# Performance work log

Measured on AMD Instinct MI355X. Metric: run time of the kernel, lower is better.

## Reference

```python
import jax, jax.numpy as jnp
import numpy as np

NEG_SLOPE = 0.2  # PyG GATConv default leaky_relu slope

N_NODES = 50000
N_EDGES = 800000
IN_DIM = 128
HID = 32
HEADS = 4


def setup_inputs() -> dict:
    key = jax.random.key(0)
    ks = jax.random.split(key, 12)
    x = jax.random.normal(ks[0], (N_NODES, IN_DIM), dtype=jnp.float32)
    edge_index = jax.random.randint(ks[1], (2, N_EDGES), 0, N_NODES, dtype=jnp.int64)
    s1 = 1.0 / np.sqrt(IN_DIM)
    s2 = 1.0 / np.sqrt(HID * HEADS)
    return {
        "x": x,
        "edge_index": edge_index,
        # layer 1: GATConv(IN_DIM -> HID, heads=HEADS, concat=True)
        "W1": jax.random.normal(ks[2], (IN_DIM, HEADS * HID), dtype=jnp.float32) * s1,
        "a_src1": jax.random.normal(ks[3], (HEADS, HID), dtype=jnp.float32) * s1,
        "a_dst1": jax.random.normal(ks[4], (HEADS, HID), dtype=jnp.float32) * s1,
        "b1": jnp.zeros((HEADS * HID,), dtype=jnp.float32),
        # head: GATConv(HEADS*HID -> 1, heads=1, concat=False)
        "W2": jax.random.normal(ks[5], (HEADS * HID, 1), dtype=jnp.float32) * s2,
        "a_src2": jax.random.normal(ks[6], (1, 1), dtype=jnp.float32) * s2,
        "a_dst2": jax.random.normal(ks[7], (1, 1), dtype=jnp.float32) * s2,
        "b2": jnp.zeros((1,), dtype=jnp.float32),
    }


def gat_conv(x, src, dst, W, a_src, a_dst, b, heads, out_ch, concat, n_nodes):
    # linear transform -> [N, H, C]
    h = (x @ W).reshape(n_nodes, heads, out_ch)
    # per-node attention halves -> [N, H]
    alpha_s = jnp.einsum('nhc,hc->nh', h, a_src)
    alpha_d = jnp.einsum('nhc,hc->nh', h, a_dst)
    # per-edge logits (gather), leaky relu -> [E, H]
    e = jax.nn.leaky_relu(alpha_s[src] + alpha_d[dst], NEG_SLOPE)
    # segment softmax over destination neighborhoods
    m = jax.ops.segment_max(e, dst, num_segments=n_nodes)  # [N, H]
    m = jnp.where(jnp.isfinite(m), m, 0.0)
    ex = jnp.exp(e - m[dst])
    denom = jax.ops.segment_sum(ex, dst, num_segments=n_nodes)  # [N, H]
    alpha = ex / (denom[dst] + 1e-16)  # [E, H]
    # weighted scatter-aggregate of source messages
    msg = h[src] * alpha[:, :, None]  # [E, H, C]
    out = jax.ops.segment_sum(msg, dst, num_segments=n_nodes)  # [N, H, C]
    out = out.reshape(n_nodes, heads * out_ch) if concat else out.mean(axis=1)
    return out + b


def reference(x, edge_index, W1, a_src1, a_dst1, b1, W2, a_src2, a_dst2, b2):
    n = x.shape[0]
    # PyG GATConv adds self-loops by default
    loops = jnp.arange(n, dtype=edge_index.dtype)
    src = jnp.concatenate([edge_index[0], loops])
    dst = jnp.concatenate([edge_index[1], loops])
    h = gat_conv(x, src, dst, W1, a_src1, a_dst1, b1, HEADS, HID, True, n)
    h = jax.nn.elu(h)  # dropout inactive in eval mode
    out = gat_conv(h, src, dst, W2, a_src2, a_dst2, b2, 1, 1, False, n)
    return out.squeeze(-1)  # [N]
```

## Files before the change

kernel.cpp:

```cpp
#include <hip/hip_runtime.h>
#include <hip/hip_bf16.h>
#include <hip/hip_fp16.h>

#define N_NODES 50000
#define N_EDGES 800000
#define E_TOT   850000
#define GBLK 64
#define GEMM_BLOCKS 782
#define NR 196
#define EPB 4096
#define BIN_BLOCKS 208
#define SEGCAP 8192

__global__ __launch_bounds__(512) void bin_kernel(const int* __restrict__ ei,
                                                  int* __restrict__ rangeCursor,
                                                  unsigned* __restrict__ gseg) {
    __shared__ int cnt[NR];
    __shared__ int gbase[NR];
    const int tid = threadIdx.x;

    for (int i = tid; i < NR; i += 512) cnt[i] = 0;
    __syncthreads();

    int e0 = blockIdx.x * EPB + tid * 8;
    bool valid = (e0 < E_TOT);
    int src[8], dst[8], rg[8], rk[8];
    if (valid) {
        if (e0 < N_EDGES) {
            int4 a = *(const int4*)(ei + e0);
            int4 b = *(const int4*)(ei + e0 + 4);
            int4 c = *(const int4*)(ei + N_EDGES + e0);
            int4 d = *(const int4*)(ei + N_EDGES + e0 + 4);
            src[0]=a.x; src[1]=a.y; src[2]=a.z; src[3]=a.w;
            src[4]=b.x; src[5]=b.y; src[6]=b.z; src[7]=b.w;
            dst[0]=c.x; dst[1]=c.y; dst[2]=c.z; dst[3]=c.w;
            dst[4]=d.x; dst[5]=d.y; dst[6]=d.z; dst[7]=d.w;
        } else {
#pragma unroll
            for (int k = 0; k < 8; k++) { src[k] = dst[k] = e0 + k - N_EDGES; }
        }
#pragma unroll
        for (int k = 0; k < 8; k++) {
            rg[k] = dst[k] >> 8;
            rk[k] = atomicAdd(&cnt[rg[k]], 1);
        }
    }
    __syncthreads();
    for (int i = tid; i < NR; i += 512) {
        int c = cnt[i];
        gbase[i] = c ? atomicAdd(&rangeCursor[i], c) : 0;
    }
    __syncthreads();
    if (valid) {
#pragma unroll
        for (int k = 0; k < 8; k++) {
            int pos = gbase[rg[k]] + rk[k];
            if (pos < SEGCAP)
                gseg[(size_t)rg[k] * SEGCAP + pos] =
                    ((unsigned)(dst[k] & 255) << 17) | (unsigned)src[k];
        }
    }
}

__global__ __launch_bounds__(512) void fatgf_kernel(const int* __restrict__ rangeCursor,
                                                    const unsigned* __restrict__ gseg,
                                                    int* __restrict__ offs,
                                                    int* __restrict__ bucket,
                                                    const float* __restrict__ x,
                                                    const float* __restrict__ W1,
                                                    const float* __restrict__ asrc1,
                                                    const float* __restrict__ adst1,
                                                    __half* __restrict__ h1,
                                                    float* __restrict__ as1,
                                                    float* __restrict__ ad1) {
    __shared__ __align__(16) char smem[(1024 + SEGCAP) * 4];
    const int tid = threadIdx.x;

    if (blockIdx.x < NR) {
        int* rsc  = (int*)smem;
        int* cnt  = rsc + 256;
        int* csc  = cnt + 256;
        int* cur  = csc + 256;
        int* lbuf = cur + 256;
        const int r = blockIdx.x;

        if (tid < 256) rsc[tid] = (tid < NR) ? min(rangeCursor[tid], SEGCAP) : 0;
        __syncthreads();
        for (int d = 1; d < 256; d <<= 1) {
            int u = (tid < 256 && tid >= d) ? rsc[tid - d] : 0;
            __syncthreads();
            if (tid < 256) rsc[tid] += u;
            __syncthreads();
        }
        const int n = min(rangeCursor[r], SEGCAP);
        const int rbase = rsc[r] - n;
        const unsigned* __restrict__ seg = gseg + (size_t)r * SEGCAP;

        if (tid < 256) cnt[tid] = 0;
        __syncthreads();
        for (int i = tid; i < n; i += 512)
            atomicAdd(&cnt[seg[i] >> 17], 1);
        __syncthreads();
        if (tid < 256) csc[tid] = cnt[tid];
        __syncthreads();
        for (int d = 1; d < 256; d <<= 1) {
            int u = (tid < 256 && tid >= d) ? csc[tid - d] : 0;
            __syncthreads();
            if (tid < 256) csc[tid] += u;
            __syncthreads();
        }
        if (tid < 256) {
            int lofs = csc[tid] - cnt[tid];
            cur[tid] = lofs;
            int node = r * 256 + tid;
            if (node < N_NODES) offs[node] = rbase + lofs;
        }
        if (r == NR - 1 && tid == 0) offs[N_NODES] = rbase + n;
        __syncthreads();
        for (int i = tid; i < n; i += 512) {
            unsigned en = seg[i];
            int p = atomicAdd(&cur[en >> 17], 1);
            lbuf[p] = (int)(en & 0x1FFFFu);
        }
        __syncthreads();
        for (int i = tid; i < n; i += 512)
            bucket[rbase + i] = lbuf[i];
        return;
    }

    float* xs    = (float*)smem;
    float* sredA = xs + 32 * 65;
    float* sredB = sredA + 8 * 64;

    const int lane = tid & 63;
    const int w    = tid >> 6;
    const int head = __builtin_amdgcn_readfirstlane(w >> 1);
    const int ch   = __builtin_amdgcn_readfirstlane(w & 1);
    const int base = (blockIdx.x - NR) * GBLK;
    const int node = base + lane;

    const float* __restrict__ wh = W1 + head * 32 + ch * 16;

    float acc[16];
#pragma unroll
    for (int j = 0; j < 16; j++) acc[j] = 0.f;

    for (int kt = 0; kt < 4; kt++) {
        __syncthreads();
        {
            int row = tid >> 3, c4 = tid & 7;
            int n2 = base + row;
            float4 v = make_float4(0.f, 0.f, 0.f, 0.f);
            if (n2 < N_NODES)
                v = *(const float4*)(x + (size_t)n2 * 128 + kt * 32 + c4 * 4);
            xs[(c4 * 4 + 0) * 65 + row] = v.x;
            xs[(c4 * 4 + 1) * 65 + row] = v.y;
            xs[(c4 * 4 + 2) * 65 + row] = v.z;
            xs[(c4 * 4 + 3) * 65 + row] = v.w;
        }
        __syncthreads();

#pragma unroll 4
        for (int kk = 0; kk < 32; kk++) {
            float xv = xs[kk * 65 + lane];
            const float* __restrict__ wr = wh + (size_t)(kt * 32 + kk) * 128;
#pragma unroll
            for (int j = 0; j < 16; j++)
                acc[j] += xv * wr[j];
        }
    }

    if (node < N_NODES) {
        __half2 hp[8];
#pragma unroll
        for (int j = 0; j < 8; j++)
            hp[j] = __floats2half2_rn(acc[2 * j], acc[2 * j + 1]);
        float4* dst = (float4*)(h1 + (size_t)node * 128 + head * 32 + ch * 16);
        dst[0] = ((float4*)hp)[0];
        dst[1] = ((float4*)hp)[1];
    }

    float sa = 0.f, da = 0.f;
#pragma unroll
    for (int j = 0; j < 16; j++) {
        float v = acc[j];
        sa += v * asrc1[head * 32 + ch * 16 + j];
        da += v * adst1[head * 32 + ch * 16 + j];
    }
    sredA[w * 64 + lane] = sa;
    sredB[w * 64 + lane] = da;
    __syncthreads();
    if (tid < 256) {
        int hh = tid >> 6;
        int nd = base + lane;
        if (nd < N_NODES) {
            as1[nd * 4 + hh] = sredA[(hh * 2) * 64 + lane] + sredA[(hh * 2 + 1) * 64 + lane];
            ad1[nd * 4 + hh] = sredB[(hh * 2) * 64 + lane] + sredB[(hh * 2 + 1) * 64 + lane];
        }
    }
}

__global__ __launch_bounds__(256) void agg1_kernel(const __half* __restrict__ h1,
                                                   const float* __restrict__ as1,
                                                   const float* __restrict__ ad1,
                                                   const int* __restrict__ offs,
                                                   const int* __restrict__ bucket,
                                                   const float* __restrict__ b1,
                                                   const float* __restrict__ W2,
                                                   float* __restrict__ h2s) {
    __shared__ int   sbuf[4][64];
    __shared__ float exbuf[4][64][4];

    int w = threadIdx.x >> 6, l = threadIdx.x & 63;
    int node = blockIdx.x * 4 + w;
    if (node >= N_NODES) return;
    int sub = l & 15;
    int ep  = l >> 4;
    int head = sub >> 2;
    int a = offs[node];
    int deg = offs[node + 1] - a;
    float4 adv = *(const float4*)(ad1 + (size_t)node * 4);

    float c[8];
#pragma unroll
    for (int k = 0; k < 8; k++) c[k] = 0.f;
    float sx = 0.f;

    for (int base = 0; base < deg; base += 64) {
        int cd = min(deg - base, 64);
        {
            bool v = l < cd;
            int s = bucket[a + base + (v ? l : 0)];
            sbuf[w][l] = s;
            float4 asv = *(const float4*)(as1 + (size_t)s * 4);
            float e0 = asv.x + adv.x, e1 = asv.y + adv.y;
            float e2 = asv.z + adv.z, e3 = asv.w + adv.w;
            e0 = fmaxf(e0, 0.2f * e0);
            e1 = fmaxf(e1, 0.2f * e1);
            e2 = fmaxf(e2, 0.2f * e2);
            e3 = fmaxf(e3, 0.2f * e3);
            float4 exv;
            exv.x = v ? __expf(e0) : 0.f;
            exv.y = v ? __expf(e1) : 0.f;
            exv.z = v ? __expf(e2) : 0.f;
            exv.w = v ? __expf(e3) : 0.f;
            *(float4*)&exbuf[w][l][0] = exv;
        }
        __builtin_amdgcn_wave_barrier();
        for (int g = 0; g < cd; g += 4) {
            int j = g + ep;
            bool v2 = j < cd;
            int jj = v2 ? j : 0;
            int s = sbuf[w][jj];
            float ex = exbuf[w][jj][head];
            if (!v2) ex = 0.f;
            float4 hv = *(const float4*)(h1 + (size_t)s * 128 + sub * 8);
            const __half2* hh = (const __half2*)&hv;
            float2 f0 = __half22float2(hh[0]);
            float2 f1 = __half22float2(hh[1]);
            float2 f2 = __half22float2(hh[2]);
            float2 f3 = __half22float2(hh[3]);
            sx += ex;
            c[0] += ex * f0.x; c[1] += ex * f0.y;
            c[2] += ex * f1.x; c[3] += ex * f1.y;
            c[4] += ex * f2.x; c[5] += ex * f2.y;
            c[6] += ex * f3.x; c[7] += ex * f3.y;
        }
        __builtin_amdgcn_wave_barrier();
    }

#pragma unroll
    for (int k = 0; k < 8; k++) {
        c[k] += __shfl_xor(c[k], 16, 64);
        c[k] += __shfl_xor(c[k], 32, 64);
    }
    sx += __shfl_xor(sx, 16, 64);
    sx += __shfl_xor(sx, 32, 64);

    float r = 1.f / (sx + 1e-16f);
    float4 blo = ((const float4*)b1)[sub * 2];
    float4 bhi = ((const float4*)b1)[sub * 2 + 1];
    float4 wlo = ((const float4*)W2)[sub * 2];
    float4 whi = ((const float4*)W2)[sub * 2 + 1];
    float ob[8] = {blo.x, blo.y, blo.z, blo.w, bhi.x, bhi.y, bhi.z, bhi.w};
    float ow[8] = {wlo.x, wlo.y, wlo.z, wlo.w, whi.x, whi.y, whi.z, whi.w};
    float p = 0.f;
#pragma unroll
    for (int k = 0; k < 8; k++) {
        float o = c[k] * r + ob[k];
        float el = (o > 0.f) ? o : (__expf(o) - 1.f);
        p += el * ow[k];
    }
    p += __shfl_xor(p, 1, 64);
    p += __shfl_xor(p, 2, 64);
    p += __shfl_xor(p, 4, 64);
    p += __shfl_xor(p, 8, 64);
    if (l == 0) h2s[node] = p;
}

__global__ __launch_bounds__(256) void agg2_kernel(const float* __restrict__ h2s,
                                                   const int* __restrict__ offs,
                                                   const int* __restrict__ bucket,
                                                   const float* __restrict__ asrc2,
                                                   const float* __restrict__ adst2,
                                                   const float* __restrict__ b2,
                                                   float* __restrict__ out) {
    int w = threadIdx.x >> 6, l = threadIdx.x & 63;
    int node = blockIdx.x * 4 + w;
    if (node >= N_NODES) return;
    float asc = asrc2[0], adc = adst2[0], bias = b2[0];
    float adn = h2s[node] * adc;
    int a = offs[node], b = offs[node + 1];
    float sx = 0.f, sw = 0.f;
    for (int i = a + l; i < b; i += 64) {
        float hs = h2s[bucket[i]];
        float e = hs * asc + adn;
        e = fmaxf(e, 0.2f * e);
        float ex = __expf(e);
        sx += ex;
        sw += ex * hs;
    }
#pragma unroll
    for (int o = 32; o > 0; o >>= 1) {
        sx += __shfl_xor(sx, o, 64);
        sw += __shfl_xor(sw, o, 64);
    }
    if (l == 0) out[node] = sw / (sx + 1e-16f) + bias;
}


extern "C" void kernel_launch(void* const* d_in, const int* in_sizes, int n_in,
                              void* d_out, int out_size, void* d_ws, size_t ws_size,
                              hipStream_t stream) {
    const float* x     = (const float*)d_in[0];
    const int*   ei    = (const int*)d_in[1];
    const float* W1    = (const float*)d_in[2];
    const float* asrc1 = (const float*)d_in[3];
    const float* adst1 = (const float*)d_in[4];
    const float* b1    = (const float*)d_in[5];
    const float* W2    = (const float*)d_in[6];
    const float* asrc2 = (const float*)d_in[7];
    const float* adst2 = (const float*)d_in[8];
    const float* b2    = (const float*)d_in[9];
    float* out = (float*)d_out;

    char* ws = (char*)d_ws;
    size_t o = 0;
    auto alloc = [&](size_t bytes) -> void* {
        void* p = ws + o;
        o += (bytes + 255) & ~(size_t)255;
        return p;
    };
    int* offs    = (int*)alloc((size_t)(N_NODES + 1) * 4);
    int* bucket  = (int*)alloc((size_t)E_TOT * 4);
    __half* h1   = (__half*)alloc((size_t)N_NODES * 128 * 2);
    float* as1   = (float*)alloc((size_t)N_NODES * 4 * 4);
    float* ad1   = (float*)alloc((size_t)N_NODES * 4 * 4);
    float* h2s   = (float*)alloc((size_t)N_NODES * 4);
    int* rangeCursor = (int*)alloc((size_t)NR * 4);
    unsigned* gseg   = (unsigned*)alloc((size_t)NR * SEGCAP * 4);

    hipMemsetAsync(rangeCursor, 0, (size_t)NR * 4, stream);

    bin_kernel<<<BIN_BLOCKS, 512, 0, stream>>>(ei, rangeCursor, gseg);

    fatgf_kernel<<<NR + GEMM_BLOCKS, 512, 0, stream>>>(
        rangeCursor, gseg, offs, bucket,
        x, W1, asrc1, adst1, h1, as1, ad1);

    agg1_kernel<<<(N_NODES + 3) / 4, 256, 0, stream>>>(
        h1, as1, ad1, offs, bucket, b1, W2, h2s);

    agg2_kernel<<<(N_NODES + 3) / 4, 256, 0, stream>>>(
        h2s, offs, bucket, asrc2, adst2, b2, out);
}
```

Baseline: 99.04 us.

## Compute layer-1 projection with fp16 MFMA using a transposed fp16 weight copy

Replaces the scalar FP32 GEMM (x @ W1) in the fused kernel with __builtin_amdgcn_mfma_f32_32x32x16_f16 on 32-node tiles, converting x to fp16 on the fly. A transposed fp16 copy of W1 is built by extra blocks appended to the bin kernel, and results are staged in shared memory to write h1 and compute the per-head attention dots. Aims to cut ALU time of the dense projection, but rounds x and W1 to fp16 before accumulation and leaves half of each 512-thread GEMM block idle.

```diff
diff --git a/kernel.cpp b/kernel.cpp
--- a/kernel.cpp
+++ b/kernel.cpp
@@ -5,19 +5,32 @@
 #define N_NODES 50000
 #define N_EDGES 800000
 #define E_TOT   850000
-#define GBLK 64
-#define GEMM_BLOCKS 782
+#define GBLK 32
+#define GEMM_BLOCKS 1563
 #define NR 196
 #define EPB 4096
 #define BIN_BLOCKS 208
+#define WT_BLOCKS 32
 #define SEGCAP 8192
+
+typedef _Float16 half8 __attribute__((ext_vector_type(8)));
+typedef float f32x16 __attribute__((ext_vector_type(16)));
 
 __global__ __launch_bounds__(512) void bin_kernel(const int* __restrict__ ei,
                                                   int* __restrict__ rangeCursor,
-                                                  unsigned* __restrict__ gseg) {
+                                                  unsigned* __restrict__ gseg,
+                                                  const float* __restrict__ W1,
+                                                  _Float16* __restrict__ Wt) {
     __shared__ int cnt[NR];
     __shared__ int gbase[NR];
     const int tid = threadIdx.x;
+
+    if (blockIdx.x >= BIN_BLOCKS) {
+        int k = (blockIdx.x - BIN_BLOCKS) * 4 + (tid >> 7);
+        int c = tid & 127;
+        Wt[c * 128 + k] = (_Float16)W1[k * 128 + c];
+        return;
+    }
 
     for (int i = tid; i < NR; i += 512) cnt[i] = 0;
     __syncthreads();
@@ -67,7 +80,7 @@
                                                     int* __restrict__ offs,
                                                     int* __restrict__ bucket,
                                                     const float* __restrict__ x,
-                                                    const float* __restrict__ W1,
+                                                    const _Float16* __restrict__ Wt,
                                                     const float* __restrict__ asrc1,
                                                     const float* __restrict__ adst1,
                                                     __half* __restrict__ h1,
@@ -128,74 +141,70 @@
         return;
     }
 
-    float* xs    = (float*)smem;
-    float* sredA = xs + 32 * 65;
-    float* sredB = sredA + 8 * 64;
-
-    const int lane = tid & 63;
+    if (tid >= 256) return;
+
+    _Float16* hl = (_Float16*)smem;
+    const int l    = tid & 63;
     const int w    = tid >> 6;
-    const int head = __builtin_amdgcn_readfirstlane(w >> 1);
-    const int ch   = __builtin_amdgcn_readfirstlane(w & 1);
+    const int g    = l >> 5;
+    const int cl   = l & 31;
+    const int col  = 32 * w + cl;
     const int base = (blockIdx.x - NR) * GBLK;
-    const int node = base + lane;
-
-    const float* __restrict__ wh = W1 + head * 32 + ch * 16;
-
-    float acc[16];
-#pragma unroll
-    for (int j = 0; j < 16; j++) acc[j] = 0.f;
-
-    for (int kt = 0; kt < 4; kt++) {
-        __syncthreads();
-        {
-            int row = tid >> 3, c4 = tid & 7;
-            int n2 = base + row;
-            float4 v = make_float4(0.f, 0.f, 0.f, 0.f);
-            if (n2 < N_NODES)
-                v = *(const float4*)(x + (size_t)n2 * 128 + kt * 32 + c4 * 4);
-            xs[(c4 * 4 + 0) * 65 + row] = v.x;
-            xs[(c4 * 4 + 1) * 65 + row] = v.y;
-            xs[(c4 * 4 + 2) * 65 + row] = v.z;
-            xs[(c4 * 4 + 3) * 65 + row] = v.w;
-        }
-        __syncthreads();
-
-#pragma unroll 4
-        for (int kk = 0; kk < 32; kk++) {
-            float xv = xs[kk * 65 + lane];
-            const float* __restrict__ wr = wh + (size_t)(kt * 32 + kk) * 128;
-#pragma unroll
-            for (int j = 0; j < 16; j++)
-                acc[j] += xv * wr[j];
-        }
-    }
-
-    if (node < N_NODES) {
-        __half2 hp[8];
-#pragma unroll
-        for (int j = 0; j < 8; j++)
-            hp[j] = __floats2half2_rn(acc[2 * j], acc[2 * j + 1]);
-        float4* dst = (float4*)(h1 + (size_t)node * 128 + head * 32 + ch * 16);
-        dst[0] = ((float4*)hp)[0];
-        dst[1] = ((float4*)hp)[1];
-    }
-
-    float sa = 0.f, da = 0.f;
+    int r = base + cl;
+    int rc = (r < N_NODES) ? r : 0;
+
+    const half8* wt8 = (const half8*)(Wt + col * 128);
+    half8 bf0 = wt8[0 + g], bf1 = wt8[2 + g], bf2 = wt8[4 + g], bf3 = wt8[6 + g];
+    half8 bf4 = wt8[8 + g], bf5 = wt8[10 + g], bf6 = wt8[12 + g], bf7 = wt8[14 + g];
+
+    const float* xr = x + (size_t)rc * 128 + 8 * g;
+    f32x16 acc = {};
+#define GAT_MFMA_STEP(S, BF)                                                  \
+    {                                                                         \
+        float4 u0 = *(const float4*)(xr + 16 * S);                            \
+        float4 u1 = *(const float4*)(xr + 16 * S + 4);                        \
+        half8 af;                                                             \
+        af[0] = (_Float16)u0.x; af[1] = (_Float16)u0.y;                       \
+        af[2] = (_Float16)u0.z; af[3] = (_Float16)u0.w;                       \
+        af[4] = (_Float16)u1.x; af[5] = (_Float16)u1.y;                       \
+        af[6] = (_Float16)u1.z; af[7] = (_Float16)u1.w;                       \
+        acc = __builtin_amdgcn_mfma_f32_32x32x16_f16(af, BF, acc, 0, 0, 0);   \
+    }
+    GAT_MFMA_STEP(0, bf0) GAT_MFMA_STEP(1, bf1) GAT_MFMA_STEP(2, bf2)
+    GAT_MFMA_STEP(3, bf3) GAT_MFMA_STEP(4, bf4) GAT_MFMA_STEP(5, bf5)
+    GAT_MFMA_STEP(6, bf6) GAT_MFMA_STEP(7, bf7)
+#undef GAT_MFMA_STEP
+
 #pragma unroll
     for (int j = 0; j < 16; j++) {
-        float v = acc[j];
-        sa += v * asrc1[head * 32 + ch * 16 + j];
-        da += v * adst1[head * 32 + ch * 16 + j];
-    }
-    sredA[w * 64 + lane] = sa;
-    sredB[w * 64 + lane] = da;
+        int nl = (j & 3) + 8 * (j >> 2) + 4 * g;
+        hl[nl * 136 + col] = (_Float16)acc[j];
+    }
     __syncthreads();
-    if (tid < 256) {
-        int hh = tid >> 6;
-        int nd = base + lane;
-        if (nd < N_NODES) {
-            as1[nd * 4 + hh] = sredA[(hh * 2) * 64 + lane] + sredA[(hh * 2 + 1) * 64 + lane];
-            ad1[nd * 4 + hh] = sredB[(hh * 2) * 64 + lane] + sredB[(hh * 2 + 1) * 64 + lane];
+
+    {
+        int nl = tid >> 3, c8 = tid & 7;
+        int node = base + nl;
+        if (node < N_NODES) {
+            float4 v0 = *(const float4*)(hl + nl * 136 + c8 * 16);
+            float4 v1 = *(const float4*)(hl + nl * 136 + c8 * 16 + 8);
+            float4* dst = (float4*)(h1 + (size_t)node * 128 + c8 * 16);
+            dst[0] = v0;
+            dst[1] = v1;
+        }
+    }
+    {
+        int nh = tid >> 1, which = tid & 1;
+        int nl = nh & 31, head = nh >> 5;
+        int node = base + nl;
+        if (node < N_NODES) {
+            const float* av = (which ? adst1 : asrc1) + head * 32;
+            const _Float16* hp = hl + nl * 136 + head * 32;
+            float s = 0.f;
+#pragma unroll
+            for (int j = 0; j < 32; j++)
+                s += (float)hp[j] * av[j];
+            (which ? ad1 : as1)[node * 4 + head] = s;
         }
     }
 }
@@ -359,14 +368,15 @@
     float* h2s   = (float*)alloc((size_t)N_NODES * 4);
     int* rangeCursor = (int*)alloc((size_t)NR * 4);
     unsigned* gseg   = (unsigned*)alloc((size_t)NR * SEGCAP * 4);
+    _Float16* Wt     = (_Float16*)alloc((size_t)128 * 128 * 2);
 
     hipMemsetAsync(rangeCursor, 0, (size_t)NR * 4, stream);
 
-    bin_kernel<<<BIN_BLOCKS, 512, 0, stream>>>(ei, rangeCursor, gseg);
+    bin_kernel<<<BIN_BLOCKS + WT_BLOCKS, 512, 0, stream>>>(ei, rangeCursor, gseg, W1, Wt);
 
     fatgf_kernel<<<NR + GEMM_BLOCKS, 512, 0, stream>>>(
         rangeCursor, gseg, offs, bucket,
-        x, W1, asrc1, adst1, h1, as1, ad1);
+        x, Wt, asrc1, adst1, h1, as1, ad1);
 
     agg1_kernel<<<(N_NODES + 3) / 4, 256, 0, stream>>>(
         h1, as1, ad1, offs, bucket, b1, W2, h2s);
```

Result: faster. 95.21 us (-3.9%).
